# Kernel tuning notes

Hardware: AMD Instinct MI355X
Metric: run time of the kernel (lower is better)

Reference implementation:

```python
import jax, jax.numpy as jnp
import numpy as np

NUM_HEADS = 16


def setup_inputs() -> dict:
    key = jax.random.key(0)
    ks = jax.random.split(key, 7)
    B, S, H = 4, 1024, 1024
    s = 0.02
    return {
        "x": jax.random.normal(ks[0], (B, S, H), dtype=jnp.float32),
        "Wq": jax.random.normal(ks[1], (H, H), dtype=jnp.float32) * s,
        "bq": jax.random.normal(ks[2], (H,), dtype=jnp.float32) * s,
        "Wk": jax.random.normal(ks[3], (H, H), dtype=jnp.float32) * s,
        "bk": jax.random.normal(ks[4], (H,), dtype=jnp.float32) * s,
        "Wv": jax.random.normal(ks[5], (H, H), dtype=jnp.float32) * s,
        "bv": jax.random.normal(ks[6], (H,), dtype=jnp.float32) * s,
    }


def _split_heads(y, num_heads):
    # rearrange 'b s (h c) -> h b s c'
    b, s, hid = y.shape
    c = hid // num_heads
    return y.reshape(b, s, num_heads, c).transpose(2, 0, 1, 3)


def reference(x, Wq, bq, Wk, bk, Wv, bv):
    h = NUM_HEADS
    head_size = x.shape[-1] // h
    # torch Linear: y = x @ W.T + b
    q = _split_heads(x @ Wq.T + bq, h)  # [h,b,s,c]
    k = _split_heads(x @ Wk.T + bk, h)
    v = _split_heads(x @ Wv.T + bv, h)
    scores = jnp.einsum('hbfc,hbtc->hbft', q, k) / jnp.sqrt(
        jnp.asarray(head_size, x.dtype))
    patterns = jax.nn.softmax(scores, axis=-1)  # softmax over t
    # NOTE: faithful to source, contracts over f (query axis) per
    # einsum('hbft,hbfc->hbtc', patterns, value)
    av = jnp.einsum('hbft,hbfc->hbtc', patterns, v)  # [h,b,t,c]
    # rearrange 'h b s c -> b s (c h)'  (channel-major interleave)
    out = av.transpose(1, 2, 3, 0)  # [b,s,c,h]
    b, s, c, hh = out.shape
    return out.reshape(b, s, c * hh)
```

## Files before the change

kernel.cpp:

```cpp
#include <hip/hip_runtime.h>
#include <hip/hip_bf16.h>

typedef short bf16x8 __attribute__((ext_vector_type(8)));
typedef short bf16x4 __attribute__((ext_vector_type(4)));
typedef float f32x4 __attribute__((ext_vector_type(4)));
typedef unsigned short u16;

#define MFMA32(a, b, c) __builtin_amdgcn_mfma_f32_16x16x32_bf16(a, b, c, 0, 0, 0)

#if defined(__has_builtin)
#if __has_builtin(__builtin_amdgcn_mfma_f32_16x16x16bf16_1k)
#define HAVE_MFMA16 1
#define MFMA16(a, b, c) __builtin_amdgcn_mfma_f32_16x16x16bf16_1k(a, b, c, 0, 0, 0)
#endif
#endif
#ifndef HAVE_MFMA16
static __device__ inline f32x4 mfma16_asm(bf16x4 a, bf16x4 b, f32x4 c) {
    f32x4 d;
    asm volatile("v_mfma_f32_16x16x16_bf16 %0, %1, %2, %3\n\ts_nop 7\n\ts_nop 7"
                 : "=v"(d) : "v"(a), "v"(b), "v"(c));
    return d;
}
#define MFMA16(a, b, c) mfma16_asm(a, b, c)
#endif

__device__ inline float fexp2(float x) {
#if defined(__has_builtin) && __has_builtin(__builtin_amdgcn_exp2f)
    return __builtin_amdgcn_exp2f(x);
#else
    return exp2f(x);
#endif
}

__device__ inline u16 f2bf(float f) {
    unsigned u = __float_as_uint(f);
    unsigned r = (u + 0x7fffu + ((u >> 16) & 1u)) >> 16;
    return (u16)r;
}

__device__ inline float bf2f(u16 v) {
    return __uint_as_float(((unsigned)v) << 16);
}

__device__ inline void gload_lds16(const void* g, void* l) {
    __builtin_amdgcn_global_load_lds(
        (const __attribute__((address_space(1))) void*)g,
        (__attribute__((address_space(3))) void*)l, 16, 0, 0);
}

#define BARRIER() __builtin_amdgcn_s_barrier()

__device__ inline int swz(int row, int colbyte) {
    return row * 128 + (colbyte ^ ((row & 7) << 4));
}

__device__ inline void stage8k_512(const u16* __restrict__ g, int gstride,
                                   u16* lds, int tid) {
    int o = tid * 16;
    int row = o >> 7;
    int colb = (o & 127) ^ ((row & 7) << 4);
    gload_lds16(g + row * gstride + (colb >> 1), (char*)lds + o);
}

__device__ inline void stage16k_256(const u16* __restrict__ g, int gstride,
                                    u16* lds, int tid) {
#pragma unroll
    for (int j = 0; j < 4; j++) {
        int o = (tid + j * 256) * 16;
        int row = o >> 7;
        int colb = (o & 127) ^ ((row & 7) << 4);
        gload_lds16(g + row * gstride + (colb >> 1), (char*)lds + o);
    }
}

__global__ void k_convert(const float* __restrict__ src, u16* __restrict__ dst, int n) {
    int i = (blockIdx.x * blockDim.x + threadIdx.x) * 4;
    if (i < n) {
        float4 v = *reinterpret_cast<const float4*>(src + i);
        ushort4 o;
        o.x = f2bf(v.x); o.y = f2bf(v.y); o.z = f2bf(v.z); o.w = f2bf(v.w);
        *reinterpret_cast<ushort4*>(dst + i) = o;
    }
}

__global__ void k_convert3(const float* __restrict__ s0, const float* __restrict__ s1,
                           const float* __restrict__ s2, u16* __restrict__ dst) {
    const float* s = (blockIdx.y == 0) ? s0 : ((blockIdx.y == 1) ? s1 : s2);
    int i = (blockIdx.x * blockDim.x + threadIdx.x) * 4;
    float4 v = *reinterpret_cast<const float4*>(s + i);
    ushort4 o;
    o.x = f2bf(v.x); o.y = f2bf(v.y); o.z = f2bf(v.z); o.w = f2bf(v.w);
    *reinterpret_cast<ushort4*>(dst + blockIdx.y * 1048576 + i) = o;
}

__global__ __launch_bounds__(256, 3) void k_proj(
    const u16* __restrict__ xb, const u16* __restrict__ wb,
    const float* __restrict__ bq, const float* __restrict__ bk, const float* __restrict__ bv,
    u16* __restrict__ outQ, u16* __restrict__ outK, u16* __restrict__ outVt)
{
    __shared__ __align__(16) u16 As[8192];
    __shared__ __align__(16) u16 Bs[8192];
    const int tid = threadIdx.x;
    const int lane = tid & 63;
    const int w = tid >> 6;
    const int bid = blockIdx.x;
    const int xcd = bid & 7, idx = bid >> 3;
    const int mg = xcd & 3, ng = xcd >> 2;
    const int m0 = (mg * 8 + (idx & 7)) * 128;
    const int nfull = ng * 12 + (idx >> 3);
    const int widx = nfull >> 3;
    const int n0 = (nfull & 7) * 128;
    const u16* W = wb + widx * 1024 * 1024;
    const float* bias = (widx == 0) ? bq : ((widx == 1) ? bk : bv);

    const int wm = (w >> 1) * 64, wn = (w & 1) * 64;
    const int lm = lane & 15, lg = lane >> 4;

    f32x4 zero = {0.f, 0.f, 0.f, 0.f};
    f32x4 acc[4][4];
#pragma unroll
    for (int m = 0; m < 4; m++)
#pragma unroll
        for (int n = 0; n < 4; n++) acc[m][n] = zero;

    for (int it = 0; it < 16; ++it) {
        stage16k_256(xb + m0 * 1024 + it * 64, 1024, As, tid);
        stage16k_256(W + n0 * 1024 + it * 64, 1024, Bs, tid);
        __syncthreads();
        const char* Ab = (const char*)As;
        const char* Bb = (const char*)Bs;
#pragma unroll
        for (int kk = 0; kk < 2; kk++) {
            bf16x8 a[4], b[4];
#pragma unroll
            for (int m = 0; m < 4; m++)
                a[m] = *(const bf16x8*)(Ab + swz(wm + m * 16 + lm, kk * 64 + lg * 16));
#pragma unroll
            for (int n = 0; n < 4; n++)
                b[n] = *(const bf16x8*)(Bb + swz(wn + n * 16 + lm, kk * 64 + lg * 16));
#pragma unroll
            for (int m = 0; m < 4; m++)
#pragma unroll
                for (int n = 0; n < 4; n++)
                    acc[m][n] = MFMA32(a[m], b[n], acc[m][n]);
        }
        __syncthreads();
    }

#pragma unroll
    for (int n = 0; n < 4; n++) {
        int col = n0 + wn + n * 16 + lm;
        float bz = bias[col];
        int h = col >> 6, c = col & 63;
#pragma unroll
        for (int m = 0; m < 4; m++) {
#pragma unroll
            for (int r = 0; r < 4; r++) {
                int row = m0 + wm + m * 16 + lg * 4 + r;
                float v = acc[m][n][r] + bz;
                int bb = row >> 10, s = row & 1023;
                int hb = h * 4 + bb;
                if (widx == 0) {
                    outQ[(hb * 1024 + s) * 64 + c] = f2bf(v * 0.18033688011112042f);
                } else if (widx == 1) {
                    outK[(hb * 1024 + s) * 64 + c] = f2bf(v);
                } else {
                    outVt[(hb * 64 + c) * 1024 + s] = f2bf(v);
                }
            }
        }
    }
}

__global__ __launch_bounds__(512, 2) void k_stats(
    const u16* __restrict__ Q, const u16* __restrict__ K, float* __restrict__ linv_out)
{
    __shared__ __align__(16) u16 sK[2][4096];
    const int bid = blockIdx.x;
    const int hb = (bid & 7) * 8 + ((bid >> 3) & 7);
    const int fb = (bid >> 6) * 256;
    const int tid = threadIdx.x, lane = tid & 63, w = tid >> 6;
    const int lm = lane & 15, lg = lane >> 4;
    const u16* Qh = Q + hb * 65536;
    const u16* Kh = K + hb * 65536;

    bf16x8 a[2][2];
#pragma unroll
    for (int fg = 0; fg < 2; fg++) {
        const u16* qp = &Qh[(fb + w * 32 + fg * 16 + lm) * 64 + lg * 8];
        a[fg][0] = *(const bf16x8*)qp;
        a[fg][1] = *(const bf16x8*)(qp + 32);
    }

    float lrun[2][4] = {{0.f, 0.f, 0.f, 0.f}, {0.f, 0.f, 0.f, 0.f}};

    stage8k_512(Kh, 64, sK[0], tid);
    int cur = 0;
    for (int it = 0; it < 16; ++it) {
        if (it < 15) {
            stage8k_512(Kh + (it + 1) * 64 * 64, 64, sK[cur ^ 1], tid);
            asm volatile("s_waitcnt vmcnt(1)" ::: "memory");
        } else {
            asm volatile("s_waitcnt vmcnt(0)" ::: "memory");
        }
        BARRIER();
        const char* base = (const char*)sK[cur];
#pragma unroll
        for (int n = 0; n < 4; n++) {
            int r = n * 16 + lm;
            bf16x8 b0 = *(const bf16x8*)(base + swz(r, lg * 16));
            bf16x8 b1 = *(const bf16x8*)(base + swz(r, 64 + lg * 16));
#pragma unroll
            for (int fg = 0; fg < 2; fg++) {
                f32x4 z = {0.f, 0.f, 0.f, 0.f};
                z = MFMA32(a[fg][0], b0, z);
                z = MFMA32(a[fg][1], b1, z);
                lrun[fg][0] += fexp2(z[0]);
                lrun[fg][1] += fexp2(z[1]);
                lrun[fg][2] += fexp2(z[2]);
                lrun[fg][3] += fexp2(z[3]);
            }
        }
        BARRIER();
        cur ^= 1;
    }
#pragma unroll
    for (int fg = 0; fg < 2; fg++) {
#pragma unroll
        for (int r = 0; r < 4; r++) {
            float s = lrun[fg][r];
            s += __shfl_xor(s, 1);
            s += __shfl_xor(s, 2);
            s += __shfl_xor(s, 4);
            s += __shfl_xor(s, 8);
            if (lm == 0)
                linv_out[hb * 1024 + fb + w * 32 + fg * 16 + lg * 4 + r] = 1.0f / s;
        }
    }
}

__global__ __launch_bounds__(512, 2) void k_av(
    const u16* __restrict__ Q, const u16* __restrict__ K, const u16* __restrict__ Vt,
    const float* __restrict__ linv, u16* __restrict__ av_sb)
{
    __shared__ __align__(16) u16 sQ[2][4096];
    __shared__ __align__(16) u16 sV[2][4096];
    __shared__ __align__(16) float linv_lds[1024];
    const int bid = blockIdx.x;
    const int hb = (bid & 7) * 8 + ((bid >> 3) & 7);
    const int tb = (bid >> 6) * 256;
    const int tid = threadIdx.x, lane = tid & 63, w = tid >> 6;
    const int lm = lane & 15, lg = lane >> 4;
    const u16* Qh = Q + hb * 65536;
    const u16* Kh = K + hb * 65536;
    const u16* Vh = Vt + hb * 65536;
    const float* lh = linv + hb * 1024;

    bf16x8 bK[2][2];
#pragma unroll
    for (int tg = 0; tg < 2; tg++) {
        const u16* kp = &Kh[(tb + w * 32 + tg * 16 + lm) * 64 + lg * 8];
        bK[tg][0] = *(const bf16x8*)kp;
        bK[tg][1] = *(const bf16x8*)(kp + 32);
    }

    f32x4 zero = {0.f, 0.f, 0.f, 0.f};
    f32x4 accv[2][4];
#pragma unroll
    for (int tg = 0; tg < 2; tg++)
#pragma unroll
        for (int m = 0; m < 4; m++) accv[tg][m] = zero;

    stage8k_512(Qh, 64, sQ[0], tid);
    stage8k_512(Vh, 1024, sV[0], tid);
    *reinterpret_cast<float2*>(&linv_lds[tid * 2]) =
        *reinterpret_cast<const float2*>(&lh[tid * 2]);
    __syncthreads();

    int cur = 0;
    for (int it = 0; it < 16; ++it) {
        if (it < 15) {
            int fn = (it + 1) * 64;
            stage8k_512(Qh + fn * 64, 64, sQ[cur ^ 1], tid);
            stage8k_512(Vh + fn, 1024, sV[cur ^ 1], tid);
            asm volatile("s_waitcnt vmcnt(2)" ::: "memory");
        } else {
            asm volatile("s_waitcnt vmcnt(0)" ::: "memory");
        }
        if (it > 0) BARRIER();
        const char* Qb = (const char*)sQ[cur];
        const char* Vb = (const char*)sV[cur];
        const int fc = it * 64;

        bf16x4 afrag[2][4];
#pragma unroll
        for (int mq = 0; mq < 4; mq++) {
            bf16x8 aq0 = *(const bf16x8*)(Qb + swz(mq * 16 + lm, lg * 16));
            bf16x8 aq1 = *(const bf16x8*)(Qb + swz(mq * 16 + lm, 64 + lg * 16));
            float4 lv = *reinterpret_cast<const float4*>(&linv_lds[fc + mq * 16 + lg * 4]);
#pragma unroll
            for (int tg = 0; tg < 2; tg++) {
                f32x4 z = {0.f, 0.f, 0.f, 0.f};
                z = MFMA32(aq0, bK[tg][0], z);
                z = MFMA32(aq1, bK[tg][1], z);
                union { __hip_bfloat162 h2[2]; bf16x4 v4; } u;
                u.h2[0] = __float22bfloat162_rn(
                    make_float2(fexp2(z[0]) * lv.x, fexp2(z[1]) * lv.y));
                u.h2[1] = __float22bfloat162_rn(
                    make_float2(fexp2(z[2]) * lv.z, fexp2(z[3]) * lv.w));
                afrag[tg][mq] = u.v4;
            }
        }
#pragma unroll
        for (int m = 0; m < 4; m++) {
#pragma unroll
            for (int kc = 0; kc < 4; kc++) {
                bf16x4 bv = *(const bf16x4*)(Vb + swz(m * 16 + lm, kc * 32 + lg * 8));
#pragma unroll
                for (int tg = 0; tg < 2; tg++)
                    accv[tg][m] = MFMA16(afrag[tg][kc], bv, accv[tg][m]);
            }
        }
        BARRIER();
        cur ^= 1;
    }

#pragma unroll
    for (int tg = 0; tg < 2; tg++) {
#pragma unroll
        for (int m = 0; m < 4; m++) {
#pragma unroll
            for (int r = 0; r < 4; r++) {
                int t = tb + w * 32 + tg * 16 + lg * 4 + r;
                av_sb[hb * 65536 + t * 64 + m * 16 + lm] = f2bf(accv[tg][m][r]);
            }
        }
    }
}

__global__ __launch_bounds__(256) void k_interleave(
    const u16* __restrict__ av_sb, float* __restrict__ out)
{
    const int bid = blockIdx.x;
    const int bb = bid >> 7, ts = (bid & 127) * 8;
    const int c = threadIdx.x & 63, tl = threadIdx.x >> 6;
#pragma unroll
    for (int p = 0; p < 2; p++) {
        int t = ts + p * 4 + tl;
        float4 w[4];
#pragma unroll
        for (int q = 0; q < 4; q++) {
#pragma unroll
            for (int j = 0; j < 4; j++) {
                int h = q * 4 + j;
                ((float*)&w[q])[j] = bf2f(av_sb[((h * 4 + bb) * 1024 + t) * 64 + c]);
            }
        }
        float4* dst = (float4*)&out[(bb * 1024 + t) * 1024 + c * 16];
        dst[0] = w[0]; dst[1] = w[1]; dst[2] = w[2]; dst[3] = w[3];
    }
}

extern "C" void kernel_launch(void* const* d_in, const int* in_sizes, int n_in,
                              void* d_out, int out_size, void* d_ws, size_t ws_size,
                              hipStream_t stream) {
    const float* x  = (const float*)d_in[0];
    const float* Wq = (const float*)d_in[1];
    const float* bq = (const float*)d_in[2];
    const float* Wk = (const float*)d_in[3];
    const float* bk = (const float*)d_in[4];
    const float* Wv = (const float*)d_in[5];
    const float* bv = (const float*)d_in[6];
    float* out = (float*)d_out;
    char* ws = (char*)d_ws;

    u16* xb = (u16*)ws;
    u16* wb = (u16*)(ws + (8u << 20));
    u16* Qb = (u16*)(ws + (14u << 20));
    u16* Kb = (u16*)(ws + (22u << 20));
    u16* Vt = (u16*)(ws + (30u << 20));
    float* linv = (float*)(ws + (38u << 20));
    u16* av_sb = (u16*)ws;

    k_convert<<<4096, 256, 0, stream>>>(x, xb, 4096 * 1024);
    k_convert3<<<dim3(1024, 3), 256, 0, stream>>>(Wq, Wk, Wv, wb);
    k_proj<<<768, 256, 0, stream>>>(xb, wb, bq, bk, bv, Qb, Kb, Vt);
    k_stats<<<256, 512, 0, stream>>>(Qb, Kb, linv);
    k_av<<<256, 512, 0, stream>>>(Qb, Kb, Vt, linv, av_sb);
    k_interleave<<<512, 256, 0, stream>>>(av_sb, out);
}
```

Before: 103.8 us.

## Double-buffer projection GEMM with BK=32 stages and raise MFMA priority

The projection GEMM moves from a single 64-wide K tile with two syncthreads per iteration to a double-buffered 32-wide K tile. The next tile's global-to-LDS loads are issued before computing on the current one, with explicit vmcnt waits, and a narrower swizzle is used for the 64-byte rows. LDS per block stays the same, and launch bounds ask for 4 blocks per CU. s_setprio is also raised around the MFMA loops in both the projection and the attention kernels. The cost is twice as many barriers per K, and the higher occupancy target may put pressure on registers.

```diff
diff --git a/kernel.cpp b/kernel.cpp
--- a/kernel.cpp
+++ b/kernel.cpp
@@ -54,6 +54,10 @@
     return row * 128 + (colbyte ^ ((row & 7) << 4));
 }
 
+__device__ inline int swz32(int row, int colbyte) {
+    return row * 64 + (colbyte ^ ((row & 3) << 4));
+}
+
 __device__ inline void stage8k_512(const u16* __restrict__ g, int gstride,
                                    u16* lds, int tid) {
     int o = tid * 16;
@@ -62,13 +66,13 @@
     gload_lds16(g + row * gstride + (colb >> 1), (char*)lds + o);
 }
 
-__device__ inline void stage16k_256(const u16* __restrict__ g, int gstride,
-                                    u16* lds, int tid) {
-#pragma unroll
-    for (int j = 0; j < 4; j++) {
+__device__ inline void stage8k32_256(const u16* __restrict__ g, int gstride,
+                                     u16* lds, int tid) {
+#pragma unroll
+    for (int j = 0; j < 2; j++) {
         int o = (tid + j * 256) * 16;
-        int row = o >> 7;
-        int colb = (o & 127) ^ ((row & 7) << 4);
+        int row = o >> 6;
+        int colb = (o & 63) ^ ((row & 3) << 4);
         gload_lds16(g + row * gstride + (colb >> 1), (char*)lds + o);
     }
 }
@@ -93,13 +97,13 @@
     *reinterpret_cast<ushort4*>(dst + blockIdx.y * 1048576 + i) = o;
 }
 
-__global__ __launch_bounds__(256, 3) void k_proj(
+__global__ __launch_bounds__(256, 4) void k_proj(
     const u16* __restrict__ xb, const u16* __restrict__ wb,
     const float* __restrict__ bq, const float* __restrict__ bk, const float* __restrict__ bv,
     u16* __restrict__ outQ, u16* __restrict__ outK, u16* __restrict__ outVt)
 {
-    __shared__ __align__(16) u16 As[8192];
-    __shared__ __align__(16) u16 Bs[8192];
+    __shared__ __align__(16) u16 As[2][4096];
+    __shared__ __align__(16) u16 Bs[2][4096];
     const int tid = threadIdx.x;
     const int lane = tid & 63;
     const int w = tid >> 6;
@@ -123,28 +127,37 @@
 #pragma unroll
         for (int n = 0; n < 4; n++) acc[m][n] = zero;
 
-    for (int it = 0; it < 16; ++it) {
-        stage16k_256(xb + m0 * 1024 + it * 64, 1024, As, tid);
-        stage16k_256(W + n0 * 1024 + it * 64, 1024, Bs, tid);
-        __syncthreads();
-        const char* Ab = (const char*)As;
-        const char* Bb = (const char*)Bs;
-#pragma unroll
-        for (int kk = 0; kk < 2; kk++) {
-            bf16x8 a[4], b[4];
-#pragma unroll
-            for (int m = 0; m < 4; m++)
-                a[m] = *(const bf16x8*)(Ab + swz(wm + m * 16 + lm, kk * 64 + lg * 16));
+    stage8k32_256(xb + m0 * 1024, 1024, As[0], tid);
+    stage8k32_256(W + n0 * 1024, 1024, Bs[0], tid);
+
+    int cur = 0;
+    for (int it = 0; it < 32; ++it) {
+        if (it < 31) {
+            stage8k32_256(xb + m0 * 1024 + (it + 1) * 32, 1024, As[cur ^ 1], tid);
+            stage8k32_256(W + n0 * 1024 + (it + 1) * 32, 1024, Bs[cur ^ 1], tid);
+            asm volatile("s_waitcnt vmcnt(4)" ::: "memory");
+        } else {
+            asm volatile("s_waitcnt vmcnt(0)" ::: "memory");
+        }
+        BARRIER();
+        const char* Ab = (const char*)As[cur];
+        const char* Bb = (const char*)Bs[cur];
+        bf16x8 a[4], b[4];
+#pragma unroll
+        for (int m = 0; m < 4; m++)
+            a[m] = *(const bf16x8*)(Ab + swz32(wm + m * 16 + lm, lg * 16));
+#pragma unroll
+        for (int n = 0; n < 4; n++)
+            b[n] = *(const bf16x8*)(Bb + swz32(wn + n * 16 + lm, lg * 16));
+        __builtin_amdgcn_s_setprio(1);
+#pragma unroll
+        for (int m = 0; m < 4; m++)
 #pragma unroll
             for (int n = 0; n < 4; n++)
-                b[n] = *(const bf16x8*)(Bb + swz(wn + n * 16 + lm, kk * 64 + lg * 16));
-#pragma unroll
-            for (int m = 0; m < 4; m++)
-#pragma unroll
-                for (int n = 0; n < 4; n++)
-                    acc[m][n] = MFMA32(a[m], b[n], acc[m][n]);
-        }
-        __syncthreads();
+                acc[m][n] = MFMA32(a[m], b[n], acc[m][n]);
+        __builtin_amdgcn_s_setprio(0);
+        BARRIER();
+        cur ^= 1;
     }
 
 #pragma unroll
@@ -311,6 +324,7 @@
                 afrag[tg][mq] = u.v4;
             }
         }
+        __builtin_amdgcn_s_setprio(1);
 #pragma unroll
         for (int m = 0; m < 4; m++) {
 #pragma unroll
@@ -321,6 +335,7 @@
                     accv[tg][m] = MFMA16(afrag[tg][kc], bv, accv[tg][m]);
             }
         }
+        __builtin_amdgcn_s_setprio(0);
         BARRIER();
         cur ^= 1;
     }
```

Measured after the change: 111.9 us. 1.08x slower.
